# Kernel tuning notes

Measured on AMD Instinct MI355X. Metric: run time of the kernel, lower is better.

## Reference

```python
import jax, jax.numpy as jnp
import numpy as np

B, T, V, E, H, D1 = 4096, 255, 32000, 64, 64, 32

def setup_inputs() -> dict:
    key = jax.random.key(0)
    ks = jax.random.split(key, 6)
    return {
        "input_diffs": jax.random.randint(ks[0], (B, T), 0, V, dtype=jnp.int32),
        "embeddings": jax.random.normal(ks[1], (V, E), dtype=jnp.float32) * 0.1,
        "Wx": jax.random.normal(ks[2], (E, 4 * H), dtype=jnp.float32) * 0.1,
        "Wh": jax.random.normal(ks[3], (H, 4 * H), dtype=jnp.float32) * 0.1,
        "b_lstm": jnp.zeros((4 * H,), dtype=jnp.float32),
        "W1": jax.random.normal(ks[4], (E, D1), dtype=jnp.float32) * 0.1,
        "b1": jnp.zeros((D1,), dtype=jnp.float32),
        "W2": jax.random.normal(ks[5], (D1, V), dtype=jnp.float32) * 0.02,
        "b2": jnp.zeros((V,), dtype=jnp.float32),
    }

def _lstm_last(emb, Wx, Wh, b):
    # emb: [B, T, E] -> scan over time; Keras gate order i, f, c(g), o
    h0 = jnp.zeros((emb.shape[0], H), dtype=emb.dtype)
    c0 = jnp.zeros_like(h0)
    def step(carry, xt):
        h, c = carry
        z = xt @ Wx + h @ Wh + b                    # [B, 4H]
        i, f, g, o = jnp.split(z, 4, axis=-1)
        i = jax.nn.sigmoid(i); f = jax.nn.sigmoid(f)
        g = jnp.tanh(g);       o = jax.nn.sigmoid(o)
        c = f * c + i * g
        h = o * jnp.tanh(c)
        return (h, c), None
    (h, _), _ = jax.lax.scan(step, (h0, c0), jnp.swapaxes(emb, 0, 1))
    return h  # [B, H] (return_sequences=False)

def reference(input_diffs, embeddings, Wx, Wh, b_lstm, W1, b1, W2, b2):
    emb = embeddings[input_diffs]                   # [B, T, E] embedding lookup
    h = _lstm_last(emb, Wx, Wh, b_lstm)             # [B, H]
    out = jax.nn.relu(h @ W1 + b1)                  # [B, 32]
    logits = out @ W2 + b2                          # [B, V]
    return jax.nn.softmax(logits, axis=-1)
```

## Files before the change

kernel.cpp:

```cpp
#include <hip/hip_runtime.h>
#include <hip/hip_bf16.h>

#define B_  4096
#define T_  255
#define V_  32000
#define E_  64
#define H_  64
#define D1_ 32

#define NCT           2000
#define NCHUNK        10
#define CT_PER_CHUNK  200
#define CT_PER_WAVE   50

typedef __attribute__((ext_vector_type(8))) short bf16x8;
typedef __attribute__((ext_vector_type(4))) float f32x4;

__device__ __forceinline__ ushort f2bf(float f) {
    __hip_bfloat16 h = __float2bfloat16(f);
    return *reinterpret_cast<ushort*>(&h);
}
__device__ __forceinline__ float fast_sigmoid(float x) {
    return __builtin_amdgcn_rcpf(1.f + __expf(-x));
}
__device__ __forceinline__ float fast_tanh(float x) {
    return 1.f - 2.f * __builtin_amdgcn_rcpf(1.f + __expf(2.f * x));
}

__device__ __forceinline__ int hswz(int row, int colb) {
    return row * 128 + (colb ^ ((row & 7) << 4));
}

__global__ __launch_bounds__(256)
void prep_kernel(const float* __restrict__ emb, ushort* __restrict__ emb_bf,
                 const float* __restrict__ W2,  ushort* __restrict__ w2p)
{
    if (blockIdx.x < 1000) {
        int i = blockIdx.x * 256 + threadIdx.x;
        const float4 a = ((const float4*)emb)[i * 2];
        const float4 b = ((const float4*)emb)[i * 2 + 1];
        ushort t[8] = { f2bf(a.x), f2bf(a.y), f2bf(a.z), f2bf(a.w),
                        f2bf(b.x), f2bf(b.y), f2bf(b.z), f2bf(b.w) };
        *(ushort4*)(&emb_bf[i * 8])     = *(ushort4*)(&t[0]);
        *(ushort4*)(&emb_bf[i * 8 + 4]) = *(ushort4*)(&t[4]);
    } else {
        int t = (blockIdx.x - 1000) * 256 + threadIdx.x;
        if (t >= NCT * 64) return;
        int ct = t >> 6, l = t & 63;
        int kbase = (l >> 4) * 8, c = ct * 16 + (l & 15);
        ushort tmp[8];
        #pragma unroll
        for (int i = 0; i < 8; ++i)
            tmp[i] = f2bf(W2[(kbase + i) * V_ + c]);
        *(ushort4*)(&w2p[t * 8])     = *(ushort4*)(&tmp[0]);
        *(ushort4*)(&w2p[t * 8 + 4]) = *(ushort4*)(&tmp[4]);
    }
}

__global__ __launch_bounds__(256)
void lstm_mfma_kernel(const int* __restrict__ idx,
                      const ushort* __restrict__ emb_bf,
                      const float* __restrict__ Wx,
                      const float* __restrict__ Wh,
                      const float* __restrict__ b,
                      float* __restrict__ h_out)
{
    __shared__ __align__(16) char hbuf[2][2048];
    __shared__ int idxs[16 * 257];

    const int tid  = threadIdx.x;
    const int lane = tid & 63;
    const int w    = tid >> 6;
    const int r0   = blockIdx.x * 16;
    const int lrow = lane & 15;
    const int lhi  = lane >> 4;
    const int jcol = w * 16 + lrow;

    bf16x8 bw[16];
    float bias[4];
    #pragma unroll
    for (int g = 0; g < 4; ++g) {
        const int col = g * 64 + jcol;
        bias[g] = b[col];
        #pragma unroll
        for (int s = 0; s < 4; ++s) {
            bf16x8 f;
            #pragma unroll
            for (int i = 0; i < 8; ++i) {
                int k = s * 32 + lhi * 8 + i;
                float v = (k < 64) ? Wx[k * 256 + col] : Wh[(k - 64) * 256 + col];
                f[i] = (short)f2bf(v);
            }
            bw[g * 4 + s] = f;
        }
    }

    {
        const int row = tid >> 4, tc = tid & 15;
        #pragma unroll
        for (int k = 0; k < 16; ++k) {
            int t = k * 16 + tc;
            if (t < T_) idxs[row * 257 + t] = idx[(r0 + row) * T_ + t];
        }
        ((float2*)hbuf[0])[tid] = make_float2(0.f, 0.f);
    }
    __syncthreads();

    f32x4 zxe[4], zxo[4];
    bf16x8 xe0, xe1, xo0, xo1;
    {
        int iv = idxs[lrow * 257 + 0];
        bf16x8 a0 = *(const bf16x8*)(emb_bf + iv * 64 + lhi * 8);
        bf16x8 a1 = *(const bf16x8*)(emb_bf + iv * 64 + 32 + lhi * 8);
        #pragma unroll
        for (int g = 0; g < 4; ++g) {
            zxe[g] = (f32x4){bias[g], bias[g], bias[g], bias[g]};
            zxe[g] = __builtin_amdgcn_mfma_f32_16x16x32_bf16(a0, bw[g * 4 + 0], zxe[g], 0, 0, 0);
            zxe[g] = __builtin_amdgcn_mfma_f32_16x16x32_bf16(a1, bw[g * 4 + 1], zxe[g], 0, 0, 0);
        }
        iv = idxs[lrow * 257 + 1];
        a0 = *(const bf16x8*)(emb_bf + iv * 64 + lhi * 8);
        a1 = *(const bf16x8*)(emb_bf + iv * 64 + 32 + lhi * 8);
        #pragma unroll
        for (int g = 0; g < 4; ++g) {
            zxo[g] = (f32x4){bias[g], bias[g], bias[g], bias[g]};
            zxo[g] = __builtin_amdgcn_mfma_f32_16x16x32_bf16(a0, bw[g * 4 + 0], zxo[g], 0, 0, 0);
            zxo[g] = __builtin_amdgcn_mfma_f32_16x16x32_bf16(a1, bw[g * 4 + 1], zxo[g], 0, 0, 0);
        }
        iv = idxs[lrow * 257 + 2];
        xe0 = *(const bf16x8*)(emb_bf + iv * 64 + lhi * 8);
        xe1 = *(const bf16x8*)(emb_bf + iv * 64 + 32 + lhi * 8);
        iv = idxs[lrow * 257 + 3];
        xo0 = *(const bf16x8*)(emb_bf + iv * 64 + lhi * 8);
        xo1 = *(const bf16x8*)(emb_bf + iv * 64 + 32 + lhi * 8);
    }

    float cst[4]  = {0.f, 0.f, 0.f, 0.f};
    float hreg[4] = {0.f, 0.f, 0.f, 0.f};

    auto do_step = [&](int t, f32x4* zx, bf16x8& x0, bf16x8& x1) {
        const int p = t & 1;
        bf16x8 ah2 = *(const bf16x8*)(&hbuf[p][hswz(lrow, lhi * 16)]);
        bf16x8 ah3 = *(const bf16x8*)(&hbuf[p][hswz(lrow, 64 + lhi * 16)]);

        f32x4 z[4];
        #pragma unroll
        for (int g = 0; g < 4; ++g)
            z[g] = __builtin_amdgcn_mfma_f32_16x16x32_bf16(ah2, bw[g * 4 + 2], zx[g], 0, 0, 0);
        #pragma unroll
        for (int g = 0; g < 4; ++g)
            z[g] = __builtin_amdgcn_mfma_f32_16x16x32_bf16(ah3, bw[g * 4 + 3], z[g], 0, 0, 0);

        if (t + 2 < T_) {
            #pragma unroll
            for (int g = 0; g < 4; ++g) {
                zx[g] = (f32x4){bias[g], bias[g], bias[g], bias[g]};
                zx[g] = __builtin_amdgcn_mfma_f32_16x16x32_bf16(x0, bw[g * 4 + 0], zx[g], 0, 0, 0);
                zx[g] = __builtin_amdgcn_mfma_f32_16x16x32_bf16(x1, bw[g * 4 + 1], zx[g], 0, 0, 0);
            }
        }
        if (t + 4 < T_) {
            int iv = idxs[lrow * 257 + (t + 4)];
            x0 = *(const bf16x8*)(emb_bf + iv * 64 + lhi * 8);
            x1 = *(const bf16x8*)(emb_bf + iv * 64 + 32 + lhi * 8);
        }

        #pragma unroll
        for (int r = 0; r < 4; ++r) {
            float cn = fast_sigmoid(z[1][r]) * cst[r]
                     + fast_sigmoid(z[0][r]) * fast_tanh(z[2][r]);
            cst[r] = cn;
            float hn = fast_sigmoid(z[3][r]) * fast_tanh(cn);
            hreg[r] = hn;
            const int row = lhi * 4 + r;
            *(ushort*)(&hbuf[p ^ 1][hswz(row, 2 * jcol)]) = f2bf(hn);
        }

        asm volatile("s_waitcnt lgkmcnt(0)\n\ts_barrier" ::: "memory");
    };

    for (int t = 0; t + 1 < T_; t += 2) {
        do_step(t,     zxe, xe0, xe1);
        do_step(t + 1, zxo, xo0, xo1);
    }
    do_step(T_ - 1, zxe, xe0, xe1);

    #pragma unroll
    for (int r = 0; r < 4; ++r)
        h_out[(r0 + lhi * 4 + r) * H_ + jcol] = hreg[r];
}

__global__ __launch_bounds__(256)
void head1_kernel(const float* __restrict__ h,
                  const float* __restrict__ W1,
                  const float* __restrict__ b1,
                  ushort* __restrict__ out32bf)
{
    int i = blockIdx.x * 256 + threadIdx.x;
    int r = i >> 5, d = i & 31;
    float a = b1[d];
    #pragma unroll
    for (int k = 0; k < 64; ++k)
        a = fmaf(h[r * H_ + k], W1[k * D1_ + d], a);
    out32bf[i] = f2bf(fmaxf(a, 0.f));
}

template <int PASS>
__global__ __launch_bounds__(256)
void head2_mfma_kernel(const ushort* __restrict__ out32bf,
                       const ushort* __restrict__ w2p,
                       const float* __restrict__ b2,
                       float* __restrict__ partial,
                       float* __restrict__ out)
{
    __shared__ float red[4][16];
    __shared__ float sinvs[16];

    const int tid  = threadIdx.x;
    const int lane = tid & 63;
    const int w    = tid >> 6;
    const int lrow = lane & 15;
    const int lhi  = lane >> 4;
    const int r0    = blockIdx.x * 16;
    const int chunk = blockIdx.y;

    if (PASS == 2) {
        if (tid < 16) {
            float s = 0.f;
            #pragma unroll
            for (int c = 0; c < NCHUNK; ++c) s += partial[(r0 + tid) * NCHUNK + c];
            sinvs[tid] = 1.f / s;
        }
        __syncthreads();
    }

    const bf16x8 A = *(const bf16x8*)(out32bf + (r0 + lrow) * D1_ + lhi * 8);

    float sacc[4] = {0.f, 0.f, 0.f, 0.f};
    float si[4];
    if (PASS == 2) {
        #pragma unroll
        for (int r = 0; r < 4; ++r) si[r] = sinvs[lhi * 4 + r];
    }

    const int ct0 = chunk * CT_PER_CHUNK + w * CT_PER_WAVE;
    for (int i = 0; i < CT_PER_WAVE; ++i) {
        const int ct = ct0 + i;
        const bf16x8 Bf = *(const bf16x8*)(w2p + ct * 512 + lane * 8);
        f32x4 z = __builtin_amdgcn_mfma_f32_16x16x32_bf16(A, Bf, (f32x4){0.f, 0.f, 0.f, 0.f}, 0, 0, 0);
        const float b2v = b2[ct * 16 + lrow];
        #pragma unroll
        for (int r = 0; r < 4; ++r) {
            float e = __expf(z[r] + b2v);
            if (PASS == 1) sacc[r] += e;
            else out[(size_t)(r0 + lhi * 4 + r) * V_ + ct * 16 + lrow] = e * si[r];
        }
    }

    if (PASS == 1) {
        #pragma unroll
        for (int r = 0; r < 4; ++r) {
            float v = sacc[r];
            #pragma unroll
            for (int off = 1; off < 16; off <<= 1) v += __shfl_xor(v, off, 16);
            if (lrow == 0) red[w][lhi * 4 + r] = v;
        }
        __syncthreads();
        if (tid < 16)
            partial[(r0 + tid) * NCHUNK + chunk] =
                red[0][tid] + red[1][tid] + red[2][tid] + red[3][tid];
    }
}

extern "C" void kernel_launch(void* const* d_in, const int* in_sizes, int n_in,
                              void* d_out, int out_size, void* d_ws, size_t ws_size,
                              hipStream_t stream)
{
    (void)in_sizes; (void)n_in; (void)out_size; (void)ws_size;

    const int*   idx = (const int*)  d_in[0];
    const float* emb = (const float*)d_in[1];
    const float* Wx  = (const float*)d_in[2];
    const float* Wh  = (const float*)d_in[3];
    const float* bl  = (const float*)d_in[4];
    const float* W1  = (const float*)d_in[5];
    const float* b1  = (const float*)d_in[6];
    const float* W2  = (const float*)d_in[7];
    const float* b2  = (const float*)d_in[8];
    float* out = (float*)d_out;

    float*  ws      = (float*)d_ws;
    float*  h       = ws;
    ushort* out32bf = (ushort*)(ws + 262144);
    ushort* w2p     = (ushort*)(ws + 262144 + 65536);
    float*  part    = ws + 262144 + 65536 + 512000;
    ushort* emb_bf  = (ushort*)(ws + 262144 + 65536 + 512000 + 40960);

    prep_kernel<<<1500, 256, 0, stream>>>(emb, emb_bf, W2, w2p);
    lstm_mfma_kernel<<<256, 256, 0, stream>>>(idx, emb_bf, Wx, Wh, bl, h);
    head1_kernel<<<(B_ * D1_) / 256, 256, 0, stream>>>(h, W1, b1, out32bf);

    dim3 g3(B_ / 16, NCHUNK);
    head2_mfma_kernel<1><<<g3, 256, 0, stream>>>(out32bf, w2p, b2, part, out);
    head2_mfma_kernel<2><<<g3, 256, 0, stream>>>(out32bf, w2p, b2, part, out);
}
```

Before: 360.1 us.

## Fuse dense1 head into LSTM kernel and compute input projection inline per step

Folds the h@W1+b1 ReLU head into the end of the LSTM kernel using an MFMA on the final hidden state in LDS, removing a separate kernel and the global h buffer. The input projection x@Wx is now computed inside each step rather than precomputed two steps ahead, freeing accumulator registers but placing more MFMAs in the serial recurrence. The g-gate weights and bias are prescaled by 2 so tanh skips a multiply.

Result: faster. 338.9 us (-5.9%).

```diff
diff --git a/kernel.cpp b/kernel.cpp
--- a/kernel.cpp
+++ b/kernel.cpp
@@ -22,6 +22,9 @@
 }
 __device__ __forceinline__ float fast_sigmoid(float x) {
     return __builtin_amdgcn_rcpf(1.f + __expf(-x));
+}
+__device__ __forceinline__ float fast_tanh_pre(float y) {
+    return 1.f - 2.f * __builtin_amdgcn_rcpf(1.f + __expf(y));
 }
 __device__ __forceinline__ float fast_tanh(float x) {
     return 1.f - 2.f * __builtin_amdgcn_rcpf(1.f + __expf(2.f * x));
@@ -63,7 +66,9 @@
                       const float* __restrict__ Wx,
                       const float* __restrict__ Wh,
                       const float* __restrict__ b,
-                      float* __restrict__ h_out)
+                      const float* __restrict__ W1,
+                      const float* __restrict__ b1,
+                      ushort* __restrict__ out32bf)
 {
     __shared__ __align__(16) char hbuf[2][2048];
     __shared__ int idxs[16 * 257];
@@ -77,11 +82,13 @@
     const int jcol = w * 16 + lrow;
 
     bf16x8 bw[16];
-    float bias[4];
+    f32x4 bsp[4];
     #pragma unroll
     for (int g = 0; g < 4; ++g) {
         const int col = g * 64 + jcol;
-        bias[g] = b[col];
+        const float sc = (g == 2) ? 2.f : 1.f;
+        const float bv = b[col] * sc;
+        bsp[g] = (f32x4){bv, bv, bv, bv};
         #pragma unroll
         for (int s = 0; s < 4; ++s) {
             bf16x8 f;
@@ -89,9 +96,24 @@
             for (int i = 0; i < 8; ++i) {
                 int k = s * 32 + lhi * 8 + i;
                 float v = (k < 64) ? Wx[k * 256 + col] : Wh[(k - 64) * 256 + col];
-                f[i] = (short)f2bf(v);
+                f[i] = (short)f2bf(v * sc);
             }
             bw[g * 4 + s] = f;
+        }
+    }
+
+    bf16x8 bw1[2];
+    float b1v = 0.f;
+    if (w < 2) {
+        const int col = w * 16 + lrow;
+        b1v = b1[col];
+        #pragma unroll
+        for (int s = 0; s < 2; ++s) {
+            bf16x8 f;
+            #pragma unroll
+            for (int i = 0; i < 8; ++i)
+                f[i] = (short)f2bf(W1[(s * 32 + lhi * 8 + i) * D1_ + col]);
+            bw1[s] = f;
         }
     }
 
@@ -106,39 +128,19 @@
     }
     __syncthreads();
 
-    f32x4 zxe[4], zxo[4];
     bf16x8 xe0, xe1, xo0, xo1;
     {
         int iv = idxs[lrow * 257 + 0];
-        bf16x8 a0 = *(const bf16x8*)(emb_bf + iv * 64 + lhi * 8);
-        bf16x8 a1 = *(const bf16x8*)(emb_bf + iv * 64 + 32 + lhi * 8);
-        #pragma unroll
-        for (int g = 0; g < 4; ++g) {
-            zxe[g] = (f32x4){bias[g], bias[g], bias[g], bias[g]};
-            zxe[g] = __builtin_amdgcn_mfma_f32_16x16x32_bf16(a0, bw[g * 4 + 0], zxe[g], 0, 0, 0);
-            zxe[g] = __builtin_amdgcn_mfma_f32_16x16x32_bf16(a1, bw[g * 4 + 1], zxe[g], 0, 0, 0);
-        }
-        iv = idxs[lrow * 257 + 1];
-        a0 = *(const bf16x8*)(emb_bf + iv * 64 + lhi * 8);
-        a1 = *(const bf16x8*)(emb_bf + iv * 64 + 32 + lhi * 8);
-        #pragma unroll
-        for (int g = 0; g < 4; ++g) {
-            zxo[g] = (f32x4){bias[g], bias[g], bias[g], bias[g]};
-            zxo[g] = __builtin_amdgcn_mfma_f32_16x16x32_bf16(a0, bw[g * 4 + 0], zxo[g], 0, 0, 0);
-            zxo[g] = __builtin_amdgcn_mfma_f32_16x16x32_bf16(a1, bw[g * 4 + 1], zxo[g], 0, 0, 0);
-        }
-        iv = idxs[lrow * 257 + 2];
         xe0 = *(const bf16x8*)(emb_bf + iv * 64 + lhi * 8);
         xe1 = *(const bf16x8*)(emb_bf + iv * 64 + 32 + lhi * 8);
-        iv = idxs[lrow * 257 + 3];
+        iv = idxs[lrow * 257 + 1];
         xo0 = *(const bf16x8*)(emb_bf + iv * 64 + lhi * 8);
         xo1 = *(const bf16x8*)(emb_bf + iv * 64 + 32 + lhi * 8);
     }
 
     float cst[4]  = {0.f, 0.f, 0.f, 0.f};
-    float hreg[4] = {0.f, 0.f, 0.f, 0.f};
-
-    auto do_step = [&](int t, f32x4* zx, bf16x8& x0, bf16x8& x1) {
+
+    auto do_step = [&](int t, bf16x8& x0, bf16x8& x1) {
         const int p = t & 1;
         bf16x8 ah2 = *(const bf16x8*)(&hbuf[p][hswz(lrow, lhi * 16)]);
         bf16x8 ah3 = *(const bf16x8*)(&hbuf[p][hswz(lrow, 64 + lhi * 16)]);
@@ -146,21 +148,19 @@
         f32x4 z[4];
         #pragma unroll
         for (int g = 0; g < 4; ++g)
-            z[g] = __builtin_amdgcn_mfma_f32_16x16x32_bf16(ah2, bw[g * 4 + 2], zx[g], 0, 0, 0);
+            z[g] = __builtin_amdgcn_mfma_f32_16x16x32_bf16(x0, bw[g * 4 + 0], bsp[g], 0, 0, 0);
+        #pragma unroll
+        for (int g = 0; g < 4; ++g)
+            z[g] = __builtin_amdgcn_mfma_f32_16x16x32_bf16(x1, bw[g * 4 + 1], z[g], 0, 0, 0);
+        #pragma unroll
+        for (int g = 0; g < 4; ++g)
+            z[g] = __builtin_amdgcn_mfma_f32_16x16x32_bf16(ah2, bw[g * 4 + 2], z[g], 0, 0, 0);
         #pragma unroll
         for (int g = 0; g < 4; ++g)
             z[g] = __builtin_amdgcn_mfma_f32_16x16x32_bf16(ah3, bw[g * 4 + 3], z[g], 0, 0, 0);
 
         if (t + 2 < T_) {
-            #pragma unroll
-            for (int g = 0; g < 4; ++g) {
-                zx[g] = (f32x4){bias[g], bias[g], bias[g], bias[g]};
-                zx[g] = __builtin_amdgcn_mfma_f32_16x16x32_bf16(x0, bw[g * 4 + 0], zx[g], 0, 0, 0);
-                zx[g] = __builtin_amdgcn_mfma_f32_16x16x32_bf16(x1, bw[g * 4 + 1], zx[g], 0, 0, 0);
-            }
-        }
-        if (t + 4 < T_) {
-            int iv = idxs[lrow * 257 + (t + 4)];
+            int iv = idxs[lrow * 257 + (t + 2)];
             x0 = *(const bf16x8*)(emb_bf + iv * 64 + lhi * 8);
             x1 = *(const bf16x8*)(emb_bf + iv * 64 + 32 + lhi * 8);
         }
@@ -168,10 +168,9 @@
         #pragma unroll
         for (int r = 0; r < 4; ++r) {
             float cn = fast_sigmoid(z[1][r]) * cst[r]
-                     + fast_sigmoid(z[0][r]) * fast_tanh(z[2][r]);
+                     + fast_sigmoid(z[0][r]) * fast_tanh_pre(z[2][r]);
             cst[r] = cn;
             float hn = fast_sigmoid(z[3][r]) * fast_tanh(cn);
-            hreg[r] = hn;
             const int row = lhi * 4 + r;
             *(ushort*)(&hbuf[p ^ 1][hswz(row, 2 * jcol)]) = f2bf(hn);
         }
@@ -180,29 +179,22 @@
     };
 
     for (int t = 0; t + 1 < T_; t += 2) {
-        do_step(t,     zxe, xe0, xe1);
-        do_step(t + 1, zxo, xo0, xo1);
-    }
-    do_step(T_ - 1, zxe, xe0, xe1);
-
-    #pragma unroll
-    for (int r = 0; r < 4; ++r)
-        h_out[(r0 + lhi * 4 + r) * H_ + jcol] = hreg[r];
-}
-
-__global__ __launch_bounds__(256)
-void head1_kernel(const float* __restrict__ h,
-                  const float* __restrict__ W1,
-                  const float* __restrict__ b1,
-                  ushort* __restrict__ out32bf)
-{
-    int i = blockIdx.x * 256 + threadIdx.x;
-    int r = i >> 5, d = i & 31;
-    float a = b1[d];
-    #pragma unroll
-    for (int k = 0; k < 64; ++k)
-        a = fmaf(h[r * H_ + k], W1[k * D1_ + d], a);
-    out32bf[i] = f2bf(fmaxf(a, 0.f));
+        do_step(t,     xe0, xe1);
+        do_step(t + 1, xo0, xo1);
+    }
+    do_step(T_ - 1, xe0, xe1);
+
+    if (w < 2) {
+        bf16x8 e0 = *(const bf16x8*)(&hbuf[1][hswz(lrow, lhi * 16)]);
+        bf16x8 e1 = *(const bf16x8*)(&hbuf[1][hswz(lrow, 64 + lhi * 16)]);
+        f32x4 zz = (f32x4){b1v, b1v, b1v, b1v};
+        zz = __builtin_amdgcn_mfma_f32_16x16x32_bf16(e0, bw1[0], zz, 0, 0, 0);
+        zz = __builtin_amdgcn_mfma_f32_16x16x32_bf16(e1, bw1[1], zz, 0, 0, 0);
+        #pragma unroll
+        for (int r = 0; r < 4; ++r)
+            out32bf[(r0 + lhi * 4 + r) * D1_ + w * 16 + lrow] =
+                f2bf(fmaxf(zz[r], 0.f));
+    }
 }
 
 template <int PASS>
@@ -290,15 +282,13 @@
     float* out = (float*)d_out;
 
     float*  ws      = (float*)d_ws;
-    float*  h       = ws;
-    ushort* out32bf = (ushort*)(ws + 262144);
-    ushort* w2p     = (ushort*)(ws + 262144 + 65536);
-    float*  part    = ws + 262144 + 65536 + 512000;
-    ushort* emb_bf  = (ushort*)(ws + 262144 + 65536 + 512000 + 40960);
+    ushort* out32bf = (ushort*)ws;
+    ushort* w2p     = (ushort*)(ws + 65536);
+    float*  part    = ws + 65536 + 512000;
+    ushort* emb_bf  = (ushort*)(ws + 65536 + 512000 + 40960);
 
     prep_kernel<<<1500, 256, 0, stream>>>(emb, emb_bf, W2, w2p);
-    lstm_mfma_kernel<<<256, 256, 0, stream>>>(idx, emb_bf, Wx, Wh, bl, h);
-    head1_kernel<<<(B_ * D1_) / 256, 256, 0, stream>>>(h, W1, b1, out32bf);
+    lstm_mfma_kernel<<<256, 256, 0, stream>>>(idx, emb_bf, Wx, Wh, bl, W1, b1, out32bf);
 
     dim3 g3(B_ / 16, NCHUNK);
     head2_mfma_kernel<1><<<g3, 256, 0, stream>>>(out32bf, w2p, b2, part, out);
```
